# Kernel optimization log

Measured on AMD Instinct MI355X. Metric: run time of the kernel, lower is better.

The kernel has to match this reference:

```python
import jax, jax.numpy as jnp
import numpy as np

B, T, C, H = 4, 2048, 768, 12
D = C // H


def setup_inputs() -> dict:
    key = jax.random.key(0)
    ks = jax.random.split(key, 7)
    s = 0.02
    return {
        "q": jax.random.normal(ks[0], (B, T, C), jnp.float32),
        "k": jax.random.normal(ks[1], (B, T, C), jnp.float32),
        "v": jax.random.normal(ks[2], (B, T, C), jnp.float32),
        "w_q": jax.random.normal(ks[3], (C, C), jnp.float32) * s,
        "w_k": jax.random.normal(ks[4], (C, C), jnp.float32) * s,
        "w_v": jax.random.normal(ks[5], (C, C), jnp.float32) * s,
        "w_o": jax.random.normal(ks[6], (C, C), jnp.float32) * s,
    }


def reference(q, k, v, w_q, w_k, w_v, w_o):
    # Linear projections (torch Linear: x @ W^T, bias=False)
    qh = (q @ w_q.T).reshape(B, T, H, D).transpose(0, 2, 1, 3)  # [B,H,T,D]
    kh = (k @ w_k.T).reshape(B, T, H, D).transpose(0, 2, 1, 3)
    vh = (v @ w_v.T).reshape(B, T, H, D).transpose(0, 2, 1, 3)
    scale = 1.0 / jnp.sqrt(jnp.asarray(D, qh.dtype))
    att = jnp.einsum("bhqd,bhkd->bhqk", qh, kh) * scale  # [B,H,T,T]
    causal = jnp.tril(jnp.ones((T, T), bool))
    att = jnp.where(causal[None, None], att, -jnp.inf)
    att = jax.nn.softmax(att, axis=-1)
    y = jnp.einsum("bhqk,bhkd->bhqd", att, vh)  # [B,H,T,D]
    y = y.transpose(0, 2, 1, 3).reshape(B, T, C)
    return y @ w_o.T
```

## Files before the change

### kernel.cpp

```cpp
#include <hip/hip_runtime.h>

#define BB 4
#define TT 2048
#define CC 768
#define HH 12
#define DD 64
#define MM (BB * TT)

#define QSCALE 0.18033688011112042f

typedef __attribute__((ext_vector_type(8))) __bf16 bf16x8;
typedef __attribute__((ext_vector_type(4))) __bf16 bf16x4;
typedef __attribute__((ext_vector_type(4))) float f32x4;

__device__ inline void gload16(const void* g, void* l) {
  __builtin_amdgcn_global_load_lds(
      (const __attribute__((address_space(1))) unsigned int*)g,
      (__attribute__((address_space(3))) unsigned int*)l, 16, 0, 0);
}

__device__ inline void cast_body(const float* __restrict__ s, __bf16* __restrict__ d) {
  long i = ((long)blockIdx.x * 256 + threadIdx.x) * 8;
  f32x4 a = *(const f32x4*)(s + i);
  f32x4 b = *(const f32x4*)(s + i + 4);
  bf16x8 o;
  o[0] = (__bf16)a[0]; o[1] = (__bf16)a[1]; o[2] = (__bf16)a[2]; o[3] = (__bf16)a[3];
  o[4] = (__bf16)b[0]; o[5] = (__bf16)b[1]; o[6] = (__bf16)b[2]; o[7] = (__bf16)b[3];
  *(bf16x8*)(d + i) = o;
}

__global__ __launch_bounds__(256) void cast3(const float* __restrict__ s0, const float* __restrict__ s1,
                                             const float* __restrict__ s2,
                                             __bf16* d0, __bf16* d1, __bf16* d2) {
  const float* s = blockIdx.y == 0 ? s0 : blockIdx.y == 1 ? s1 : s2;
  __bf16* d = blockIdx.y == 0 ? d0 : blockIdx.y == 1 ? d1 : d2;
  cast_body(s, d);
}

__global__ __launch_bounds__(256) void cast4(const float* __restrict__ s0, const float* __restrict__ s1,
                                             const float* __restrict__ s2, const float* __restrict__ s3,
                                             __bf16* d0, __bf16* d1, __bf16* d2, __bf16* d3) {
  const float* s; __bf16* d;
  switch (blockIdx.y) {
    case 0: s = s0; d = d0; break;
    case 1: s = s1; d = d1; break;
    case 2: s = s2; d = d2; break;
    default: s = s3; d = d3; break;
  }
  cast_body(s, d);
}

__device__ inline void stage_tile(const __bf16* __restrict__ A, const __bf16* __restrict__ W,
                                  long m0, long n0, int k0,
                                  __bf16* As, __bf16* Bs, int wave, int lane) {
#pragma unroll
  for (int i = 0; i < 4; ++i) {
    const int r = wave + i * 4;
    const int L = r * 1024 + lane * 16;
    const int row = L >> 7;
    const int sc = (L >> 4) & 7;
    const int gc = sc ^ (row & 7);
    gload16(A + (m0 + row) * CC + k0 + gc * 8, As + r * 512);
    gload16(W + (n0 + row) * CC + k0 + gc * 8, Bs + r * 512);
  }
}

__device__ inline void compute_tile(const __bf16* As, const __bf16* Bs, f32x4 (&acc)[4][4],
                                    int wr, int wc, int l15, int g) {
#pragma unroll
  for (int kk = 0; kk < 2; ++kk) {
    bf16x8 af[4], bfr[4];
#pragma unroll
    for (int mi = 0; mi < 4; ++mi) {
      const int row = wr + mi * 16 + l15;
      const int c = (kk * 4 + g) ^ (row & 7);
      af[mi] = *(const bf16x8*)&As[row * 64 + c * 8];
    }
#pragma unroll
    for (int ni = 0; ni < 4; ++ni) {
      const int row = wc + ni * 16 + l15;
      const int c = (kk * 4 + g) ^ (row & 7);
      bfr[ni] = *(const bf16x8*)&Bs[row * 64 + c * 8];
    }
    __builtin_amdgcn_s_setprio(1);
#pragma unroll
    for (int mi = 0; mi < 4; ++mi)
#pragma unroll
      for (int ni = 0; ni < 4; ++ni)
        acc[mi][ni] = __builtin_amdgcn_mfma_f32_16x16x32_bf16(af[mi], bfr[ni], acc[mi][ni], 0, 0, 0);
    __builtin_amdgcn_s_setprio(0);
  }
}

template <int MODE>
__global__ __launch_bounds__(256) void gemm_proj(
    const __bf16* __restrict__ A0, const __bf16* __restrict__ A1, const __bf16* __restrict__ A2,
    const __bf16* __restrict__ W0, const __bf16* __restrict__ W1, const __bf16* __restrict__ W2,
    void* D0, void* D1, void* D2) {
  __shared__ __align__(16) char smem[65536];
  __bf16* As0 = (__bf16*)smem;
  __bf16* Bs0 = (__bf16*)(smem + 16384);
  __bf16* As1 = (__bf16*)(smem + 32768);
  __bf16* Bs1 = (__bf16*)(smem + 49152);

  const int id = blockIdx.x;
  const int xcd = id & 7, slot = id >> 3;
  const int n_idx = slot % 6;
  const int mzg = xcd + 8 * (slot / 6);
  const int z = (MODE == 0) ? (mzg >> 6) : 0;
  const int m_idx = (MODE == 0) ? (mzg & 63) : mzg;

  const __bf16* __restrict__ A = z == 0 ? A0 : z == 1 ? A1 : A2;
  const __bf16* __restrict__ W = z == 0 ? W0 : z == 1 ? W1 : W2;
  const long m0 = (long)m_idx * 128;
  const long n0 = (long)n_idx * 128;
  const int tid = threadIdx.x;
  const int wave = tid >> 6, lane = tid & 63;
  const int l15 = lane & 15, g = lane >> 4;
  const int wr = (wave >> 1) * 64, wc = (wave & 1) * 64;

  f32x4 acc[4][4] = {};

  stage_tile(A, W, m0, n0, 0, As0, Bs0, wave, lane);
  __syncthreads();
  for (int kt = 0; kt < 12; kt += 2) {
    stage_tile(A, W, m0, n0, (kt + 1) * 64, As1, Bs1, wave, lane);
    compute_tile(As0, Bs0, acc, wr, wc, l15, g);
    __syncthreads();
    if (kt + 2 < 12) stage_tile(A, W, m0, n0, (kt + 2) * 64, As0, Bs0, wave, lane);
    compute_tile(As1, Bs1, acc, wr, wc, l15, g);
    __syncthreads();
  }

  const int b = (int)(m0 >> 11);
  const int t0 = (int)(m0 & (TT - 1));
  if (MODE == 1) {
    float* Ef = (float*)smem;
    float* Dst = (float*)D0;
    for (int p = 0; p < 2; ++p) {
      if (p) __syncthreads();
      if ((wr >> 6) == p) {
#pragma unroll
        for (int mi = 0; mi < 4; ++mi)
#pragma unroll
          for (int ni = 0; ni < 4; ++ni)
#pragma unroll
            for (int j = 0; j < 4; ++j) {
              const int ml = mi * 16 + g * 4 + j;
              const int n = wc + ni * 16 + l15;
              *(float*)((char*)Ef + ml * 512 + ((n * 4) ^ (((ml >> 2) & 7) << 4))) = acc[mi][ni][j];
            }
      }
      __syncthreads();
#pragma unroll
      for (int sw = 0; sw < 8; ++sw) {
        const int r = sw * 8 + (tid >> 5);
        const int c = (tid & 31) * 4;
        f32x4 vv = *(const f32x4*)((char*)Ef + r * 512 + ((c * 4) ^ (((r >> 2) & 7) << 4)));
        *(f32x4*)&Dst[(m0 + p * 64 + r) * CC + n0 + c] = vv;
      }
    }
  } else {
    __bf16* Eh = (__bf16*)smem;
    __bf16* Dst = (__bf16*)(z == 0 ? D0 : z == 1 ? D1 : D2);
    for (int p = 0; p < 2; ++p) {
      if (p) __syncthreads();
      if (z != 2) {
        if ((wr >> 6) == p) {
#pragma unroll
          for (int mi = 0; mi < 4; ++mi)
#pragma unroll
            for (int ni = 0; ni < 4; ++ni)
#pragma unroll
              for (int j = 0; j < 4; ++j) {
                const int ml = mi * 16 + g * 4 + j;
                const int n = wc + ni * 16 + l15;
                float v = acc[mi][ni][j];
                if (z == 0) v *= QSCALE;
                *(__bf16*)((char*)Eh + ml * 256 + ((n * 2) ^ (((ml >> 2) & 7) << 4))) = (__bf16)v;
              }
        }
      } else {
        if ((wc >> 6) == p) {
#pragma unroll
          for (int mi = 0; mi < 4; ++mi)
#pragma unroll
            for (int ni = 0; ni < 4; ++ni)
#pragma unroll
              for (int j = 0; j < 4; ++j) {
                const int nl = ni * 16 + l15;
                const int mm = wr + mi * 16 + g * 4 + j;
                *(__bf16*)((char*)Eh + nl * 256 + ((mm * 2) ^ ((nl & 7) << 4))) = (__bf16)acc[mi][ni][j];
              }
        }
      }
      __syncthreads();
#pragma unroll
      for (int sw = 0; sw < 4; ++sw) {
        const int r = sw * 16 + (tid >> 4);
        const int c = (tid & 15) * 8;
        if (z != 2) {
          bf16x8 vv = *(const bf16x8*)((char*)Eh + r * 256 + ((c * 2) ^ (((r >> 2) & 7) << 4)));
          const int t = t0 + p * 64 + r;
          const int n = (int)n0 + c;
          const int h = n >> 6, d = n & 63;
          *(bf16x8*)&Dst[(((long)(b * HH + h)) * TT + t) * DD + d] = vv;
        } else {
          bf16x8 vv = *(const bf16x8*)((char*)Eh + r * 256 + ((c * 2) ^ ((r & 7) << 4)));
          const int n = (int)n0 + p * 64 + r;
          const int h = n >> 6, d = n & 63;
          *(bf16x8*)&Dst[(((long)(b * HH + h)) * DD + d) * TT + t0 + c] = vv;
        }
      }
    }
  }
}

__global__ __launch_bounds__(256) void attn_fwd(
    const __bf16* __restrict__ Qh, const __bf16* __restrict__ Kh,
    const __bf16* __restrict__ Vh, __bf16* __restrict__ Y) {
  __shared__ __bf16 Kl[2][64 * 64];
  __shared__ __bf16 Vl[2][64 * 64];
  __shared__ __bf16 Pl[4][16 * 64];

  const int id = blockIdx.x;
  const int xcd = id & 7, slot = id >> 3;
  const int a = slot & 15;
  const int bh = xcd + 8 * (slot >> 4);

  const int tid = threadIdx.x, wave = tid >> 6, lane = tid & 63;
  const int l15 = lane & 15, g = lane >> 4;
  const __bf16* Kbase = Kh + (long)bh * TT * DD;
  const __bf16* VTbase = Vh + (long)bh * DD * TT;
  const int b = bh / HH, h = bh % HH;
  char* Pb = (char*)&Pl[wave][0];

  const int s_a = a + 1;
  const int total = 33;

  int qt = a;
  int qrow = qt * 64 + wave * 16 + l15;
  bf16x8 qf0, qf1;
  {
    const __bf16* qptr = Qh + ((long)bh * TT + qrow) * DD;
    qf0 = *(const bf16x8*)(qptr + g * 8);
    qf1 = *(const bf16x8*)(qptr + 32 + g * 8);
  }

  f32x4 oacc[4] = {};
  float m = -1e30f, lsum = 0.f;

#pragma unroll
  for (int i = 0; i < 2; ++i) {
    const int r = wave + i * 4;
    const int L = r * 1024 + lane * 16;
    const int row = L >> 7, sc = (L >> 4) & 7, gc = sc ^ (row & 7);
    gload16(Kbase + (long)row * DD + gc * 8, &Kl[0][r * 512]);
    gload16(VTbase + (long)row * TT + gc * 8, &Vl[0][r * 512]);
  }

  for (int s = 0; s < total; ++s) {
    __syncthreads();

    if (s + 1 < total) {
      const int kt1 = (s + 1 >= s_a) ? (s + 1 - s_a) : (s + 1);
      const int kv1 = kt1 * 64;
      __bf16* Kd = Kl[(s + 1) & 1];
      __bf16* Vd = Vl[(s + 1) & 1];
#pragma unroll
      for (int i = 0; i < 2; ++i) {
        const int r = wave + i * 4;
        const int L = r * 1024 + lane * 16;
        const int row = L >> 7, sc = (L >> 4) & 7, gc = sc ^ (row & 7);
        gload16(Kbase + (long)(kv1 + row) * DD + gc * 8, Kd + r * 512);
        gload16(VTbase + (long)row * TT + kv1 + gc * 8, Vd + r * 512);
      }
    }

    if (s == s_a) {
      float lrow = lsum + __shfl_xor(lsum, 16);
      lrow += __shfl_xor(lrow, 32);
#pragma unroll
      for (int j = 0; j < 4; ++j) {
        const float inv = 1.0f / __shfl(lrow, g * 4 + j);
        const int q = qt * 64 + wave * 16 + g * 4 + j;
#pragma unroll
        for (int ni = 0; ni < 4; ++ni)
          Y[((long)(b * TT + q)) * CC + h * DD + ni * 16 + l15] = (__bf16)(oacc[ni][j] * inv);
      }
      qt = 31 - a;
      qrow = qt * 64 + wave * 16 + l15;
      const __bf16* qptr = Qh + ((long)bh * TT + qrow) * DD;
      qf0 = *(const bf16x8*)(qptr + g * 8);
      qf1 = *(const bf16x8*)(qptr + 32 + g * 8);
#pragma unroll
      for (int ni = 0; ni < 4; ++ni) oacc[ni] = (f32x4){0.f, 0.f, 0.f, 0.f};
      m = -1e30f; lsum = 0.f;
    }

    const int kt = (s >= s_a) ? (s - s_a) : s;
    const int kv0 = kt * 64;
    const bool maskt = (kt == qt);
    const __bf16* Kc = Kl[s & 1];
    const __bf16* Vc = Vl[s & 1];

    f32x4 sacc[4] = {};
    __builtin_amdgcn_s_setprio(1);
#pragma unroll
    for (int mi = 0; mi < 4; ++mi) {
      const int row = mi * 16 + l15;
      const int c0 = g ^ (row & 7);
      const int c1 = (4 + g) ^ (row & 7);
      bf16x8 kfa = *(const bf16x8*)&Kc[row * 64 + c0 * 8];
      bf16x8 kfb = *(const bf16x8*)&Kc[row * 64 + c1 * 8];
      sacc[mi] = __builtin_amdgcn_mfma_f32_16x16x32_bf16(kfa, qf0, sacc[mi], 0, 0, 0);
      sacc[mi] = __builtin_amdgcn_mfma_f32_16x16x32_bf16(kfb, qf1, sacc[mi], 0, 0, 0);
    }
    __builtin_amdgcn_s_setprio(0);

    float ps[4][4];
    float tmax = -3e30f;
    if (maskt) {
#pragma unroll
      for (int mi = 0; mi < 4; ++mi)
#pragma unroll
        for (int j = 0; j < 4; ++j) {
          float sv = sacc[mi][j];
          const int kv = kv0 + mi * 16 + g * 4 + j;
          if (kv > qrow) sv = -3e30f;
          ps[mi][j] = sv;
          tmax = fmaxf(tmax, sv);
        }
    } else {
#pragma unroll
      for (int mi = 0; mi < 4; ++mi)
#pragma unroll
        for (int j = 0; j < 4; ++j) {
          const float sv = sacc[mi][j];
          ps[mi][j] = sv;
          tmax = fmaxf(tmax, sv);
        }
    }

    if (!__all(tmax <= m + 8.0f)) {
      float full = fmaxf(tmax, __shfl_xor(tmax, 16));
      full = fmaxf(full, __shfl_xor(full, 32));
      const float mnew = fmaxf(m, full);
      const float corr = __builtin_amdgcn_exp2f(m - mnew);
#pragma unroll
      for (int j = 0; j < 4; ++j) {
        const float cj = __shfl(corr, g * 4 + j);
#pragma unroll
        for (int ni = 0; ni < 4; ++ni) oacc[ni][j] *= cj;
      }
      lsum *= corr;
      m = mnew;
    }

#pragma unroll
    for (int mi = 0; mi < 4; ++mi) {
      bf16x4 pv;
#pragma unroll
      for (int j = 0; j < 4; ++j) {
        const float p = __builtin_amdgcn_exp2f(ps[mi][j] - m);
        lsum += p;
        pv[j] = (__bf16)p;
      }
      *(bf16x4*)(Pb + l15 * 128 + ((mi * 32 + g * 8) ^ ((l15 & 7) << 4))) = pv;
    }

    __builtin_amdgcn_s_setprio(1);
#pragma unroll
    for (int ks = 0; ks < 2; ++ks) {
      bf16x8 pa = *(const bf16x8*)(Pb + l15 * 128 + ((ks * 64 + g * 16) ^ ((l15 & 7) << 4)));
#pragma unroll
      for (int ni = 0; ni < 4; ++ni) {
        const int d = ni * 16 + l15;
        const int c = (ks * 4 + g) ^ (d & 7);
        bf16x8 vf = *(const bf16x8*)&Vc[d * 64 + c * 8];
        oacc[ni] = __builtin_amdgcn_mfma_f32_16x16x32_bf16(pa, vf, oacc[ni], 0, 0, 0);
      }
    }
    __builtin_amdgcn_s_setprio(0);
  }

  {
    float lrow = lsum + __shfl_xor(lsum, 16);
    lrow += __shfl_xor(lrow, 32);
#pragma unroll
    for (int j = 0; j < 4; ++j) {
      const float inv = 1.0f / __shfl(lrow, g * 4 + j);
      const int q = qt * 64 + wave * 16 + g * 4 + j;
#pragma unroll
      for (int ni = 0; ni < 4; ++ni)
        Y[((long)(b * TT + q)) * CC + h * DD + ni * 16 + l15] = (__bf16)(oacc[ni][j] * inv);
    }
  }
}

extern "C" void kernel_launch(void* const* d_in, const int* in_sizes, int n_in,
                              void* d_out, int out_size, void* d_ws, size_t ws_size,
                              hipStream_t stream) {
  (void)in_sizes; (void)n_in; (void)out_size; (void)ws_size;
  const float* q  = (const float*)d_in[0];
  const float* k  = (const float*)d_in[1];
  const float* v  = (const float*)d_in[2];
  const float* wq = (const float*)d_in[3];
  const float* wk = (const float*)d_in[4];
  const float* wv = (const float*)d_in[5];
  const float* wo = (const float*)d_in[6];

  char* ws = (char*)d_ws;
  const long SZX = (long)MM * CC * 2;
  const long SZW = (long)CC * CC * 2;
  __bf16* xq  = (__bf16*)(ws);
  __bf16* xk  = (__bf16*)(ws + SZX);
  __bf16* xv  = (__bf16*)(ws + 2 * SZX);
  __bf16* wwq = (__bf16*)(ws + 3 * SZX);
  __bf16* wwk = (__bf16*)(ws + 3 * SZX + SZW);
  __bf16* wwv = (__bf16*)(ws + 3 * SZX + 2 * SZW);
  __bf16* wwo = (__bf16*)(ws + 3 * SZX + 3 * SZW);
  __bf16* qh  = (__bf16*)(ws + 3 * SZX + 4 * SZW);
  __bf16* kh  = (__bf16*)(ws + 4 * SZX + 4 * SZW);
  __bf16* vh  = (__bf16*)(ws + 5 * SZX + 4 * SZW);
  __bf16* y   = xq;

  cast3<<<dim3((MM * CC) / 2048, 3, 1), 256, 0, stream>>>(q, k, v, xq, xk, xv);
  cast4<<<dim3((CC * CC) / 2048, 4, 1), 256, 0, stream>>>(wq, wk, wv, wo, wwq, wwk, wwv, wwo);
  gemm_proj<0><<<dim3(1152, 1, 1), 256, 0, stream>>>(xq, xk, xv, wwq, wwk, wwv, qh, kh, vh);
  attn_fwd<<<dim3(768, 1, 1), 256, 0, stream>>>(qh, kh, vh, y);
  gemm_proj<1><<<dim3(384, 1, 1), 256, 0, stream>>>(y, y, y, wwo, wwo, wwo, d_out, d_out, d_out);
}
```

Before: 240.7 us.

## Merge cast kernels, single-buffer GEMM for occupancy, compute softmax row sums via MFMA

Merges the two cast launches into one kernel over a flat block range, which removes one launch. The projection GEMM drops from double-buffered to single-buffered LDS (32KB) and asks for 4 blocks per CU, trading load/compute overlap within a block for more resident blocks. In attention, the per-lane softmax denominator plus its shuffle reductions is replaced by an extra MFMA of P against a ones vector, and the row max now uses a tree reduction. The row sum is now taken from the bf16-rounded probabilities rather than fp32, which shifts accuracy slightly, and losing the GEMM prefetch could expose global-load latency.

```diff
diff --git a/kernel.cpp b/kernel.cpp
--- a/kernel.cpp
+++ b/kernel.cpp
@@ -19,35 +19,33 @@
       (__attribute__((address_space(3))) unsigned int*)l, 16, 0, 0);
 }
 
-__device__ inline void cast_body(const float* __restrict__ s, __bf16* __restrict__ d) {
-  long i = ((long)blockIdx.x * 256 + threadIdx.x) * 8;
+__global__ __launch_bounds__(256) void cast_all(
+    const float* __restrict__ q, const float* __restrict__ k, const float* __restrict__ v,
+    const float* __restrict__ wq, const float* __restrict__ wk,
+    const float* __restrict__ wv, const float* __restrict__ wo,
+    __bf16* xq, __bf16* xk, __bf16* xv,
+    __bf16* wwq, __bf16* wwk, __bf16* wwv, __bf16* wwo) {
+  const int id = blockIdx.x;
+  const float* s; __bf16* d; long base;
+  if (id < 9216) {
+    const int t = id / 3072;
+    base = (long)(id % 3072) * 2048;
+    s = t == 0 ? q : t == 1 ? k : v;
+    d = t == 0 ? xq : t == 1 ? xk : xv;
+  } else {
+    const int r = id - 9216;
+    const int t = r / 288;
+    base = (long)(r % 288) * 2048;
+    s = t == 0 ? wq : t == 1 ? wk : t == 2 ? wv : wo;
+    d = t == 0 ? wwq : t == 1 ? wwk : t == 2 ? wwv : wwo;
+  }
+  const long i = base + (long)threadIdx.x * 8;
   f32x4 a = *(const f32x4*)(s + i);
   f32x4 b = *(const f32x4*)(s + i + 4);
   bf16x8 o;
   o[0] = (__bf16)a[0]; o[1] = (__bf16)a[1]; o[2] = (__bf16)a[2]; o[3] = (__bf16)a[3];
   o[4] = (__bf16)b[0]; o[5] = (__bf16)b[1]; o[6] = (__bf16)b[2]; o[7] = (__bf16)b[3];
   *(bf16x8*)(d + i) = o;
-}
-
-__global__ __launch_bounds__(256) void cast3(const float* __restrict__ s0, const float* __restrict__ s1,
-                                             const float* __restrict__ s2,
-                                             __bf16* d0, __bf16* d1, __bf16* d2) {
-  const float* s = blockIdx.y == 0 ? s0 : blockIdx.y == 1 ? s1 : s2;
-  __bf16* d = blockIdx.y == 0 ? d0 : blockIdx.y == 1 ? d1 : d2;
-  cast_body(s, d);
-}
-
-__global__ __launch_bounds__(256) void cast4(const float* __restrict__ s0, const float* __restrict__ s1,
-                                             const float* __restrict__ s2, const float* __restrict__ s3,
-                                             __bf16* d0, __bf16* d1, __bf16* d2, __bf16* d3) {
-  const float* s; __bf16* d;
-  switch (blockIdx.y) {
-    case 0: s = s0; d = d0; break;
-    case 1: s = s1; d = d1; break;
-    case 2: s = s2; d = d2; break;
-    default: s = s3; d = d3; break;
-  }
-  cast_body(s, d);
 }
 
 __device__ inline void stage_tile(const __bf16* __restrict__ A, const __bf16* __restrict__ W,
@@ -93,15 +91,13 @@
 }
 
 template <int MODE>
-__global__ __launch_bounds__(256) void gemm_proj(
+__global__ __launch_bounds__(256, 4) void gemm_proj(
     const __bf16* __restrict__ A0, const __bf16* __restrict__ A1, const __bf16* __restrict__ A2,
     const __bf16* __restrict__ W0, const __bf16* __restrict__ W1, const __bf16* __restrict__ W2,
     void* D0, void* D1, void* D2) {
-  __shared__ __align__(16) char smem[65536];
-  __bf16* As0 = (__bf16*)smem;
-  __bf16* Bs0 = (__bf16*)(smem + 16384);
-  __bf16* As1 = (__bf16*)(smem + 32768);
-  __bf16* Bs1 = (__bf16*)(smem + 49152);
+  __shared__ __align__(16) char smem[32768];
+  __bf16* As = (__bf16*)smem;
+  __bf16* Bs = (__bf16*)(smem + 16384);
 
   const int id = blockIdx.x;
   const int xcd = id & 7, slot = id >> 3;
@@ -121,16 +117,13 @@
 
   f32x4 acc[4][4] = {};
 
-  stage_tile(A, W, m0, n0, 0, As0, Bs0, wave, lane);
+  for (int kt = 0; kt < 12; ++kt) {
+    __syncthreads();
+    stage_tile(A, W, m0, n0, kt * 64, As, Bs, wave, lane);
+    __syncthreads();
+    compute_tile(As, Bs, acc, wr, wc, l15, g);
+  }
   __syncthreads();
-  for (int kt = 0; kt < 12; kt += 2) {
-    stage_tile(A, W, m0, n0, (kt + 1) * 64, As1, Bs1, wave, lane);
-    compute_tile(As0, Bs0, acc, wr, wc, l15, g);
-    __syncthreads();
-    if (kt + 2 < 12) stage_tile(A, W, m0, n0, (kt + 2) * 64, As0, Bs0, wave, lane);
-    compute_tile(As1, Bs1, acc, wr, wc, l15, g);
-    __syncthreads();
-  }
 
   const int b = (int)(m0 >> 11);
   const int t0 = (int)(m0 & (TT - 1));
@@ -238,6 +231,10 @@
   const int s_a = a + 1;
   const int total = 33;
 
+  bf16x8 ones;
+#pragma unroll
+  for (int i = 0; i < 8; ++i) ones[i] = (__bf16)1.0f;
+
   int qt = a;
   int qrow = qt * 64 + wave * 16 + l15;
   bf16x8 qf0, qf1;
@@ -248,7 +245,8 @@
   }
 
   f32x4 oacc[4] = {};
-  float m = -1e30f, lsum = 0.f;
+  f32x4 lacc = {};
+  float m = -1e30f;
 
 #pragma unroll
   for (int i = 0; i < 2; ++i) {
@@ -278,11 +276,9 @@
     }
 
     if (s == s_a) {
-      float lrow = lsum + __shfl_xor(lsum, 16);
-      lrow += __shfl_xor(lrow, 32);
 #pragma unroll
       for (int j = 0; j < 4; ++j) {
-        const float inv = 1.0f / __shfl(lrow, g * 4 + j);
+        const float inv = 1.0f / lacc[j];
         const int q = qt * 64 + wave * 16 + g * 4 + j;
 #pragma unroll
         for (int ni = 0; ni < 4; ++ni)
@@ -295,7 +291,8 @@
       qf1 = *(const bf16x8*)(qptr + 32 + g * 8);
 #pragma unroll
       for (int ni = 0; ni < 4; ++ni) oacc[ni] = (f32x4){0.f, 0.f, 0.f, 0.f};
-      m = -1e30f; lsum = 0.f;
+      lacc = (f32x4){0.f, 0.f, 0.f, 0.f};
+      m = -1e30f;
     }
 
     const int kt = (s >= s_a) ? (s - s_a) : s;
@@ -319,28 +316,28 @@
     __builtin_amdgcn_s_setprio(0);
 
     float ps[4][4];
-    float tmax = -3e30f;
+    float tmx[4];
     if (maskt) {
 #pragma unroll
-      for (int mi = 0; mi < 4; ++mi)
+      for (int mi = 0; mi < 4; ++mi) {
 #pragma unroll
         for (int j = 0; j < 4; ++j) {
           float sv = sacc[mi][j];
           const int kv = kv0 + mi * 16 + g * 4 + j;
           if (kv > qrow) sv = -3e30f;
           ps[mi][j] = sv;
-          tmax = fmaxf(tmax, sv);
         }
+        tmx[mi] = fmaxf(fmaxf(ps[mi][0], ps[mi][1]), fmaxf(ps[mi][2], ps[mi][3]));
+      }
     } else {
 #pragma unroll
-      for (int mi = 0; mi < 4; ++mi)
-#pragma unroll
-        for (int j = 0; j < 4; ++j) {
-          const float sv = sacc[mi][j];
-          ps[mi][j] = sv;
-          tmax = fmaxf(tmax, sv);
-        }
-    }
+      for (int mi = 0; mi < 4; ++mi) {
+#pragma unroll
+        for (int j = 0; j < 4; ++j) ps[mi][j] = sacc[mi][j];
+        tmx[mi] = fmaxf(fmaxf(ps[mi][0], ps[mi][1]), fmaxf(ps[mi][2], ps[mi][3]));
+      }
+    }
+    const float tmax = fmaxf(fmaxf(tmx[0], tmx[1]), fmaxf(tmx[2], tmx[3]));
 
     if (!__all(tmax <= m + 8.0f)) {
       float full = fmaxf(tmax, __shfl_xor(tmax, 16));
@@ -350,10 +347,10 @@
 #pragma unroll
       for (int j = 0; j < 4; ++j) {
         const float cj = __shfl(corr, g * 4 + j);
+        lacc[j] *= cj;
 #pragma unroll
         for (int ni = 0; ni < 4; ++ni) oacc[ni][j] *= cj;
       }
-      lsum *= corr;
       m = mnew;
     }
 
@@ -361,11 +358,8 @@
     for (int mi = 0; mi < 4; ++mi) {
       bf16x4 pv;
 #pragma unroll
-      for (int j = 0; j < 4; ++j) {
-        const float p = __builtin_amdgcn_exp2f(ps[mi][j] - m);
-        lsum += p;
-        pv[j] = (__bf16)p;
-      }
+      for (int j = 0; j < 4; ++j)
+        pv[j] = (__bf16)__builtin_amdgcn_exp2f(ps[mi][j] - m);
       *(bf16x4*)(Pb + l15 * 128 + ((mi * 32 + g * 8) ^ ((l15 & 7) << 4))) = pv;
     }
 
@@ -373,6 +367,7 @@
 #pragma unroll
     for (int ks = 0; ks < 2; ++ks) {
       bf16x8 pa = *(const bf16x8*)(Pb + l15 * 128 + ((ks * 64 + g * 16) ^ ((l15 & 7) << 4)));
+      lacc = __builtin_amdgcn_mfma_f32_16x16x32_bf16(pa, ones, lacc, 0, 0, 0);
 #pragma unroll
       for (int ni = 0; ni < 4; ++ni) {
         const int d = ni * 16 + l15;
@@ -384,17 +379,13 @@
     __builtin_amdgcn_s_setprio(0);
   }
 
-  {
-    float lrow = lsum + __shfl_xor(lsum, 16);
-    lrow += __shfl_xor(lrow, 32);
-#pragma unroll
-    for (int j = 0; j < 4; ++j) {
-      const float inv = 1.0f / __shfl(lrow, g * 4 + j);
-      const int q = qt * 64 + wave * 16 + g * 4 + j;
-#pragma unroll
-      for (int ni = 0; ni < 4; ++ni)
-        Y[((long)(b * TT + q)) * CC + h * DD + ni * 16 + l15] = (__bf16)(oacc[ni][j] * inv);
-    }
+#pragma unroll
+  for (int j = 0; j < 4; ++j) {
+    const float inv = 1.0f / lacc[j];
+    const int q = qt * 64 + wave * 16 + g * 4 + j;
+#pragma unroll
+    for (int ni = 0; ni < 4; ++ni)
+      Y[((long)(b * TT + q)) * CC + h * DD + ni * 16 + l15] = (__bf16)(oacc[ni][j] * inv);
   }
 }
 
@@ -425,8 +416,8 @@
   __bf16* vh  = (__bf16*)(ws + 5 * SZX + 4 * SZW);
   __bf16* y   = xq;
 
-  cast3<<<dim3((MM * CC) / 2048, 3, 1), 256, 0, stream>>>(q, k, v, xq, xk, xv);
-  cast4<<<dim3((CC * CC) / 2048, 4, 1), 256, 0, stream>>>(wq, wk, wv, wo, wwq, wwk, wwv, wwo);
+  cast_all<<<dim3(10368, 1, 1), 256, 0, stream>>>(q, k, v, wq, wk, wv, wo,
+                                                  xq, xk, xv, wwq, wwk, wwv, wwo);
   gemm_proj<0><<<dim3(1152, 1, 1), 256, 0, stream>>>(xq, xk, xv, wwq, wwk, wwv, qh, kh, vh);
   attn_fwd<<<dim3(768, 1, 1), 256, 0, stream>>>(qh, kh, vh, y);
   gemm_proj<1><<<dim3(384, 1, 1), 256, 0, stream>>>(y, y, y, wwo, wwo, wwo, d_out, d_out, d_out);
```

Measured after the change: 233.5 us. 1.03x faster.
